# Performance work log

Hardware: AMD Instinct MI355X
Metric: run time of the kernel (lower is better)

The kernel has to match this reference:

```python
import jax, jax.numpy as jnp
import numpy as np

N = 50000      # nodes
E = 800000     # edges (before self-loops)
G = 64         # graphs
F_IN = 128
HID = 64
HEADS = 2
OUT = 10
NEG_SLOPE = 0.2


def setup_inputs() -> dict:
    key = jax.random.key(0)
    ks = jax.random.split(key, 12)
    x = jax.random.normal(ks[0], (N, F_IN), dtype=jnp.float32)
    edge_index = jax.random.randint(ks[1], (2, E), 0, N, dtype=jnp.int64)
    batch = jnp.sort(jax.random.randint(ks[2], (N,), 0, G, dtype=jnp.int64))
    s = 0.1
    params = {
        "W1": jax.random.normal(ks[3], (F_IN, HEADS * HID), dtype=jnp.float32) * s,
        "att_src1": jax.random.normal(ks[4], (HEADS, HID), dtype=jnp.float32) * s,
        "att_dst1": jax.random.normal(ks[5], (HEADS, HID), dtype=jnp.float32) * s,
        "b1": jnp.zeros((HEADS * HID,), dtype=jnp.float32),
        "W2": jax.random.normal(ks[6], (HEADS * HID, HEADS * HID), dtype=jnp.float32) * s,
        "att_src2": jax.random.normal(ks[7], (HEADS, HID), dtype=jnp.float32) * s,
        "att_dst2": jax.random.normal(ks[8], (HEADS, HID), dtype=jnp.float32) * s,
        "b2": jnp.zeros((HEADS * HID,), dtype=jnp.float32),
        "Wl": jax.random.normal(ks[9], (HEADS * HID, OUT), dtype=jnp.float32) * s,
        "bl": jnp.zeros((OUT,), dtype=jnp.float32),
    }
    return {"x": x, "edge_index": edge_index, "batch": batch, **params}


def gat_conv(x, W, att_src, att_dst, bias, src, dst):
    # x: [N, Fin]; W: [Fin, H*C]
    h = (x @ W).reshape(N, HEADS, HID)                      # [N, H, C]
    a_src = jnp.sum(h * att_src, axis=-1)                   # [N, H]
    a_dst = jnp.sum(h * att_dst, axis=-1)                   # [N, H]
    alpha = jax.nn.leaky_relu(a_src[src] + a_dst[dst], NEG_SLOPE)  # [Etot, H]
    # segment softmax over incoming edges of each dst node
    m = jax.ops.segment_max(alpha, dst, num_segments=N)     # [N, H]
    alpha = jnp.exp(alpha - m[dst])
    denom = jax.ops.segment_sum(alpha, dst, num_segments=N)
    alpha = alpha / (denom[dst] + 1e-16)
    out = jax.ops.segment_sum(alpha[:, :, None] * h[src], dst, num_segments=N)
    return out.reshape(N, HEADS * HID) + bias


def reference(x, edge_index, batch, W1, att_src1, att_dst1, b1,
              W2, att_src2, att_dst2, b2, Wl, bl):
    # PyG GATConv default: add self-loops
    loop = jnp.arange(N, dtype=edge_index.dtype)
    src = jnp.concatenate([edge_index[0], loop])
    dst = jnp.concatenate([edge_index[1], loop])

    h = jax.nn.relu(gat_conv(x, W1, att_src1, att_dst1, b1, src, dst))
    h = jax.nn.relu(gat_conv(h, W2, att_src2, att_dst2, b2, src, dst))

    # global_mean_pool over graphs
    sums = jax.ops.segment_sum(h, batch, num_segments=G)        # [G, H*C]
    cnts = jax.ops.segment_sum(jnp.ones((N,), h.dtype), batch, num_segments=G)
    pooled = sums / jnp.maximum(cnts, 1.0)[:, None]
    return pooled @ Wl + bl                                      # [G, OUT]
```

## Files before the change

kernel.cpp:

```cpp
#include <hip/hip_runtime.h>
#include <hip/hip_fp16.h>
#include <math.h>

#define N_NODES 50000
#define N_EDGES 800000
#define ETOT    850000
#define GRAPHS  64
#define FIN     128
#define HC      128
#define OUTF    10
#define NEG     0.2f

#define NBUCK   196
#define BCAP    8192
#define EPT     8

using half8  = __attribute__((ext_vector_type(8))) _Float16;
using float4v = __attribute__((ext_vector_type(4))) float;

__global__ void initk(int* tails, float* sums) {
    int i = blockIdx.x * 256 + threadIdx.x;
    if (i < NBUCK) tails[i] = 0;
    if (i < GRAPHS * HC) sums[i] = 0.f;
}

__global__ void wconv(const float* __restrict__ W1, const float* __restrict__ W2,
                      _Float16* __restrict__ WT1, _Float16* __restrict__ WT2) {
    int t = blockIdx.x * 256 + threadIdx.x;
    if (t < 16384) {
        int n = t >> 7, k = t & 127;
        WT1[t] = (_Float16)W1[k * 128 + n];
        WT2[t] = (_Float16)W2[k * 128 + n];
    }
}

__global__ __launch_bounds__(256) void bucketA(const int* __restrict__ ei,
                                               int* __restrict__ tails,
                                               int* __restrict__ bdata) {
    __shared__ int hist[NBUCK];
    __shared__ int lbase[NBUCK];
    int t = threadIdx.x;
    int e0 = blockIdx.x * (256 * EPT);
    for (int i = t; i < NBUCK; i += 256) hist[i] = 0;
    __syncthreads();

    int bb[EPT], pk[EPT], rk[EPT];
#pragma unroll
    for (int i = 0; i < EPT; ++i) {
        int e = e0 + i * 256 + t;
        bb[i] = -1;
        if (e < ETOT) {
            int s, d;
            if (e < N_EDGES) { s = ei[e]; d = ei[N_EDGES + e]; }
            else             { s = d = e - N_EDGES; }
            bb[i] = d >> 8;
            pk[i] = s | ((d & 255) << 16);
            rk[i] = atomicAdd(&hist[bb[i]], 1);
        }
    }
    __syncthreads();
    for (int i = t; i < NBUCK; i += 256)
        lbase[i] = atomicAdd(&tails[i], hist[i]);
    __syncthreads();
#pragma unroll
    for (int i = 0; i < EPT; ++i)
        if (bb[i] >= 0) bdata[bb[i] * BCAP + lbase[bb[i]] + rk[i]] = pk[i];
}

__global__ void scanBuckets(const int* __restrict__ tails,
                            int* __restrict__ csrBase,
                            int* __restrict__ rowptr) {
    __shared__ int sh[256];
    int t = threadIdx.x;
    int c = (t < NBUCK) ? tails[t] : 0;
    sh[t] = c;
    __syncthreads();
    for (int off = 1; off < 256; off <<= 1) {
        int add = (t >= off) ? sh[t - off] : 0;
        __syncthreads();
        sh[t] += add;
        __syncthreads();
    }
    if (t < NBUCK) csrBase[t] = sh[t] - c;
    if (t == NBUCK - 1) rowptr[N_NODES] = sh[t];
}

__global__ __launch_bounds__(256) void bucketB(const int* __restrict__ bdata,
                                               const int* __restrict__ tails,
                                               const int* __restrict__ csrBase,
                                               int* __restrict__ rowptr,
                                               int* __restrict__ csr) {
    __shared__ int hist[256];
    __shared__ int scanws[256];
    int b = blockIdx.x;
    int t = threadIdx.x;
    int nodes0 = b << 8;
    int nnodes = min(256, N_NODES - nodes0);
    int cnt  = tails[b];
    int base = csrBase[b];
    const int* bd = &bdata[b * BCAP];

    hist[t] = 0;
    __syncthreads();
    for (int j = t; j < cnt; j += 256) atomicAdd(&hist[bd[j] >> 16], 1);
    __syncthreads();
    scanws[t] = hist[t];
    __syncthreads();
    for (int off = 1; off < 256; off <<= 1) {
        int add = (t >= off) ? scanws[t - off] : 0;
        __syncthreads();
        scanws[t] += add;
        __syncthreads();
    }
    int excl = scanws[t] - hist[t];
    if (t < nnodes) rowptr[nodes0 + t] = base + excl;
    __syncthreads();
    hist[t] = excl;
    __syncthreads();
    for (int j = t; j < cnt; j += 256) {
        int pkv = bd[j];
        int pos = atomicAdd(&hist[pkv >> 16], 1);
        csr[base + pos] = pkv & 0xFFFF;
    }
}

template<bool FP32IN>
__global__ __launch_bounds__(256) void gemmMFMA(const void* __restrict__ Xin,
                                                const _Float16* __restrict__ WT,
                                                const float* __restrict__ att_s,
                                                const float* __restrict__ att_d,
                                                _Float16* __restrict__ H16,
                                                float2* __restrict__ a_src,
                                                float2* __restrict__ a_dst) {
    __shared__ _Float16 wt[128][128];
    int t = threadIdx.x;

    for (int i = t; i < 128 * 16; i += 256) {
        int n = i >> 4, ch = i & 15;
        int k0 = ch * 8;
        half8 v = *(const half8*)&WT[n * 128 + k0];
        *(half8*)&wt[n][k0 ^ ((n & 7) << 3)] = v;
    }

    int w = t >> 6, lane = t & 63;
    int hi = lane >> 4, l16 = lane & 15;
    int rbase = blockIdx.x * 64 + w * 16;
    int arow = min(rbase + l16, N_NODES - 1);

    half8 a[4];
    if (FP32IN) {
        const float* X = (const float*)Xin;
#pragma unroll
        for (int kb = 0; kb < 4; ++kb) {
            int k0 = kb * 32 + hi * 8;
            float4 x0 = *(const float4*)&X[(size_t)arow * 128 + k0];
            float4 x1 = *(const float4*)&X[(size_t)arow * 128 + k0 + 4];
            half8 v;
            v[0] = (_Float16)x0.x; v[1] = (_Float16)x0.y;
            v[2] = (_Float16)x0.z; v[3] = (_Float16)x0.w;
            v[4] = (_Float16)x1.x; v[5] = (_Float16)x1.y;
            v[6] = (_Float16)x1.z; v[7] = (_Float16)x1.w;
            a[kb] = v;
        }
    } else {
        const _Float16* X = (const _Float16*)Xin;
#pragma unroll
        for (int kb = 0; kb < 4; ++kb)
            a[kb] = *(const half8*)&X[(size_t)arow * 128 + kb * 32 + hi * 8];
    }

    __syncthreads();

    float4v acc[8];
#pragma unroll
    for (int ct = 0; ct < 8; ++ct) {
        float4v c = {0.f, 0.f, 0.f, 0.f};
        int n = ct * 16 + l16;
#pragma unroll
        for (int kb = 0; kb < 4; ++kb) {
            int k0 = (kb * 32 + hi * 8) ^ ((n & 7) << 3);
            half8 b = *(const half8*)&wt[n][k0];
            c = __builtin_amdgcn_mfma_f32_16x16x32_f16(a[kb], b, c, 0, 0, 0);
        }
        acc[ct] = c;
    }

    int grow0 = rbase + hi * 4;
#pragma unroll
    for (int ct = 0; ct < 8; ++ct) {
#pragma unroll
        for (int r = 0; r < 4; ++r) {
            int grow = grow0 + r;
            if (grow < N_NODES)
                H16[(size_t)grow * 128 + ct * 16 + l16] = (_Float16)acc[ct][r];
        }
    }

    float as_[8], ad_[8];
#pragma unroll
    for (int ct = 0; ct < 8; ++ct) {
        as_[ct] = att_s[ct * 16 + l16];
        ad_[ct] = att_d[ct * 16 + l16];
    }
#pragma unroll
    for (int r = 0; r < 4; ++r) {
        float s0 = 0.f, s1 = 0.f, d0 = 0.f, d1 = 0.f;
#pragma unroll
        for (int ct = 0; ct < 4; ++ct) { s0 += acc[ct][r] * as_[ct]; d0 += acc[ct][r] * ad_[ct]; }
#pragma unroll
        for (int ct = 4; ct < 8; ++ct) { s1 += acc[ct][r] * as_[ct]; d1 += acc[ct][r] * ad_[ct]; }
        for (int off = 1; off < 16; off <<= 1) {
            s0 += __shfl_xor(s0, off); s1 += __shfl_xor(s1, off);
            d0 += __shfl_xor(d0, off); d1 += __shfl_xor(d1, off);
        }
        int grow = grow0 + r;
        if (l16 == 0 && grow < N_NODES) {
            a_src[grow] = make_float2(s0, s1);
            a_dst[grow] = make_float2(d0, d1);
        }
    }
}

__device__ __forceinline__ float leaky(float x) { return x > 0.f ? x : NEG * x; }

__global__ __launch_bounds__(256) void aggk(const __half* __restrict__ H16,
                                            const float2* __restrict__ a_src,
                                            const float2* __restrict__ a_dst,
                                            const int* __restrict__ rowptr,
                                            const int* __restrict__ csr,
                                            const float* __restrict__ bias,
                                            float* __restrict__ outp,
                                            _Float16* __restrict__ out16) {
    int wid = (blockIdx.x * 256 + threadIdx.x) >> 6;
    int lane = threadIdx.x & 63;
    if (wid >= N_NODES) return;
    int rbeg = rowptr[wid], rend = rowptr[wid + 1];
    float2 ad = a_dst[wid];

    int grp = lane >> 4;
    int gl  = lane & 15;
    int head = gl >> 3;
    float adh = head ? ad.y : ad.x;
    int f = gl * 8;

    float acc[8] = {0.f, 0.f, 0.f, 0.f, 0.f, 0.f, 0.f, 0.f};
    float denom = 0.f;
#pragma unroll 2
    for (int j = rbeg + grp; j < rend; j += 4) {
        int s = csr[j];
        float2 as = a_src[s];
        float w = __expf(leaky((head ? as.y : as.x) + adh));
        uint4 raw = *(const uint4*)&H16[(size_t)s * 128 + f];
        float2 f0 = __half22float2(*(__half2*)&raw.x);
        float2 f1 = __half22float2(*(__half2*)&raw.y);
        float2 f2 = __half22float2(*(__half2*)&raw.z);
        float2 f3 = __half22float2(*(__half2*)&raw.w);
        acc[0] += w * f0.x; acc[1] += w * f0.y;
        acc[2] += w * f1.x; acc[3] += w * f1.y;
        acc[4] += w * f2.x; acc[5] += w * f2.y;
        acc[6] += w * f3.x; acc[7] += w * f3.y;
        denom += w;
    }
#pragma unroll
    for (int off = 16; off <= 32; off <<= 1) {
#pragma unroll
        for (int i = 0; i < 8; ++i) acc[i] += __shfl_xor(acc[i], off);
        denom += __shfl_xor(denom, off);
    }

    if (grp == 0) {
        float inv = 1.f / (denom + 1e-16f);
        float4 bb0 = *(const float4*)&bias[f];
        float4 bb1 = *(const float4*)&bias[f + 4];
        float o[8];
        o[0] = fmaxf(acc[0] * inv + bb0.x, 0.f);
        o[1] = fmaxf(acc[1] * inv + bb0.y, 0.f);
        o[2] = fmaxf(acc[2] * inv + bb0.z, 0.f);
        o[3] = fmaxf(acc[3] * inv + bb0.w, 0.f);
        o[4] = fmaxf(acc[4] * inv + bb1.x, 0.f);
        o[5] = fmaxf(acc[5] * inv + bb1.y, 0.f);
        o[6] = fmaxf(acc[6] * inv + bb1.z, 0.f);
        o[7] = fmaxf(acc[7] * inv + bb1.w, 0.f);
        *(float4*)&outp[(size_t)wid * 128 + f]     = make_float4(o[0], o[1], o[2], o[3]);
        *(float4*)&outp[(size_t)wid * 128 + f + 4] = make_float4(o[4], o[5], o[6], o[7]);
        half8 h;
#pragma unroll
        for (int i = 0; i < 8; ++i) h[i] = (_Float16)o[i];
        *(half8*)&out16[(size_t)wid * 128 + f] = h;
    }
}

__global__ void countk(const int* __restrict__ batch, int* cnt) {
    int g = threadIdx.x;
    if (g >= GRAPHS) return;
    int lo = 0, hi = N_NODES;
    while (lo < hi) { int mid = (lo + hi) >> 1; if (batch[mid] < g) lo = mid + 1; else hi = mid; }
    int lb = lo;
    lo = 0; hi = N_NODES;
    while (lo < hi) { int mid = (lo + hi) >> 1; if (batch[mid] < g + 1) lo = mid + 1; else hi = mid; }
    cnt[g] = lo - lb;
}

__global__ void poolk(const float* __restrict__ H, const int* __restrict__ batch,
                      float* __restrict__ sums) {
    int f = threadIdx.x;
    int n0 = blockIdx.x * 64;
    if (n0 >= N_NODES) return;
    int n1 = min(n0 + 64, N_NODES);
    int g = batch[n0];
    float run = 0.f;
    for (int n = n0; n < n1; ++n) {
        int gn = batch[n];
        if (gn != g) { atomicAdd(&sums[g * 128 + f], run); run = 0.f; g = gn; }
        run += H[(size_t)n * 128 + f];
    }
    atomicAdd(&sums[g * 128 + f], run);
}

__global__ void finalk(const float* __restrict__ sums, const int* __restrict__ cnt,
                       const float* __restrict__ Wl, const float* __restrict__ bl,
                       float* __restrict__ out) {
    int t = threadIdx.x;
    if (t >= GRAPHS * OUTF) return;
    int g = t / OUTF, o = t % OUTF;
    float inv = 1.f / fmaxf((float)cnt[g], 1.f);
    float acc = 0.f;
#pragma unroll 8
    for (int k = 0; k < 128; ++k) acc += sums[g * 128 + k] * Wl[k * OUTF + o];
    out[t] = acc * inv + bl[o];
}

extern "C" void kernel_launch(void* const* d_in, const int* in_sizes, int n_in,
                              void* d_out, int out_size, void* d_ws, size_t ws_size,
                              hipStream_t stream) {
    const float* x        = (const float*)d_in[0];
    const int*   ei       = (const int*)d_in[1];
    const int*   batch    = (const int*)d_in[2];
    const float* W1       = (const float*)d_in[3];
    const float* att_src1 = (const float*)d_in[4];
    const float* att_dst1 = (const float*)d_in[5];
    const float* b1       = (const float*)d_in[6];
    const float* W2       = (const float*)d_in[7];
    const float* att_src2 = (const float*)d_in[8];
    const float* att_dst2 = (const float*)d_in[9];
    const float* b2       = (const float*)d_in[10];
    const float* Wl       = (const float*)d_in[11];
    const float* bl       = (const float*)d_in[12];
    float* out = (float*)d_out;

    size_t off = 0;
    auto alloc = [&](size_t bytes) -> void* {
        void* p = (char*)d_ws + off;
        off = (off + bytes + 255) & ~(size_t)255;
        return p;
    };
    float*    B       = (float*)alloc((size_t)N_NODES * 128 * 4);
    _Float16* H16     = (_Float16*)alloc((size_t)N_NODES * 128 * 2);
    _Float16* B16     = (_Float16*)alloc((size_t)N_NODES * 128 * 2);
    _Float16* WT1     = (_Float16*)alloc(16384 * 2);
    _Float16* WT2     = (_Float16*)alloc(16384 * 2);
    float2*   a_src   = (float2*)alloc((size_t)N_NODES * 8);
    float2*   a_dst   = (float2*)alloc((size_t)N_NODES * 8);
    int*      bdata   = (int*)alloc((size_t)NBUCK * BCAP * 4);
    int*      tails   = (int*)alloc(NBUCK * 4);
    int*      csrBase = (int*)alloc(NBUCK * 4);
    int*      rowptr  = (int*)alloc((size_t)(N_NODES + 1) * 4);
    int*      csr     = (int*)alloc((size_t)ETOT * 4);
    float*    sums    = (float*)alloc((size_t)GRAPHS * HC * 4);
    int*      cnt     = (int*)alloc(GRAPHS * 4);

    initk<<<32, 256, 0, stream>>>(tails, sums);
    wconv<<<64, 256, 0, stream>>>(W1, W2, WT1, WT2);
    bucketA<<<(ETOT + 2047) / 2048, 256, 0, stream>>>(ei, tails, bdata);
    scanBuckets<<<1, 256, 0, stream>>>(tails, csrBase, rowptr);
    bucketB<<<NBUCK, 256, 0, stream>>>(bdata, tails, csrBase, rowptr, csr);

    const int gemmBlocks = (N_NODES + 63) / 64;
    const int waveBlocks = (N_NODES * 64 + 255) / 256;

    gemmMFMA<true><<<gemmBlocks, 256, 0, stream>>>(x, WT1, att_src1, att_dst1,
                                                   H16, a_src, a_dst);
    aggk<<<waveBlocks, 256, 0, stream>>>((const __half*)H16, a_src, a_dst,
                                         rowptr, csr, b1, B, B16);

    gemmMFMA<false><<<gemmBlocks, 256, 0, stream>>>(B16, WT2, att_src2, att_dst2,
                                                    H16, a_src, a_dst);
    aggk<<<waveBlocks, 256, 0, stream>>>((const __half*)H16, a_src, a_dst,
                                         rowptr, csr, b2, B, B16);

    countk<<<1, 64, 0, stream>>>(batch, cnt);
    poolk<<<(N_NODES + 63) / 64, 128, 0, stream>>>(B, batch, sums);
    finalk<<<1, 640, 0, stream>>>(sums, cnt, Wl, bl, out);
}
```

Baseline: 183.5 us.

## Drop fp32 node output, widen per-lane features, prefetch edge index in aggregation

The aggregation kernel no longer writes a float32 copy of node features; pooling now reads the fp16 buffer instead. Each lane now handles 16 features with two 16-byte loads, so 8 edges are processed in parallel per wavefront rather than 4, and the next source index is prefetched one iteration ahead. This removes 25.6 MB of fp32 writes per layer plus the matching pooling reads, and puts more edges in flight per wave. The cost is an extra shuffle-reduction stage, higher register use, and pooling now summing fp16-rounded values.

```diff
diff --git a/kernel.cpp b/kernel.cpp
--- a/kernel.cpp
+++ b/kernel.cpp
@@ -15,7 +15,7 @@
 #define BCAP    8192
 #define EPT     8
 
-using half8  = __attribute__((ext_vector_type(8))) _Float16;
+using half8   = __attribute__((ext_vector_type(8))) _Float16;
 using float4v = __attribute__((ext_vector_type(4))) float;
 
 __global__ void initk(int* tails, float* sums) {
@@ -229,7 +229,6 @@
                                             const int* __restrict__ rowptr,
                                             const int* __restrict__ csr,
                                             const float* __restrict__ bias,
-                                            float* __restrict__ outp,
                                             _Float16* __restrict__ out16) {
     int wid = (blockIdx.x * 256 + threadIdx.x) >> 6;
     int lane = threadIdx.x & 63;
@@ -237,56 +236,61 @@
     int rbeg = rowptr[wid], rend = rowptr[wid + 1];
     float2 ad = a_dst[wid];
 
-    int grp = lane >> 4;
-    int gl  = lane & 15;
-    int head = gl >> 3;
+    int grp = lane >> 3;
+    int gl  = lane & 7;
+    int head = gl >> 2;
     float adh = head ? ad.y : ad.x;
-    int f = gl * 8;
-
-    float acc[8] = {0.f, 0.f, 0.f, 0.f, 0.f, 0.f, 0.f, 0.f};
+    int f = gl * 16;
+
+    float acc[16];
+#pragma unroll
+    for (int i = 0; i < 16; ++i) acc[i] = 0.f;
     float denom = 0.f;
-#pragma unroll 2
-    for (int j = rbeg + grp; j < rend; j += 4) {
-        int s = csr[j];
+
+    int j = rbeg + grp;
+    int sNext = (j < rend) ? csr[j] : 0;
+    for (; j < rend; j += 8) {
+        int s = sNext;
+        int jn = j + 8;
+        if (jn < rend) sNext = csr[jn];
         float2 as = a_src[s];
-        float w = __expf(leaky((head ? as.y : as.x) + adh));
-        uint4 raw = *(const uint4*)&H16[(size_t)s * 128 + f];
-        float2 f0 = __half22float2(*(__half2*)&raw.x);
-        float2 f1 = __half22float2(*(__half2*)&raw.y);
-        float2 f2 = __half22float2(*(__half2*)&raw.z);
-        float2 f3 = __half22float2(*(__half2*)&raw.w);
-        acc[0] += w * f0.x; acc[1] += w * f0.y;
-        acc[2] += w * f1.x; acc[3] += w * f1.y;
-        acc[4] += w * f2.x; acc[5] += w * f2.y;
-        acc[6] += w * f3.x; acc[7] += w * f3.y;
-        denom += w;
-    }
-#pragma unroll
-    for (int off = 16; off <= 32; off <<= 1) {
-#pragma unroll
-        for (int i = 0; i < 8; ++i) acc[i] += __shfl_xor(acc[i], off);
+        float wgt = __expf(leaky((head ? as.y : as.x) + adh));
+        const uint4* hp = (const uint4*)&H16[(size_t)s * 128 + f];
+        uint4 r0 = hp[0];
+        uint4 r1 = hp[1];
+        float2 p;
+        p = __half22float2(*(__half2*)&r0.x); acc[0] += wgt * p.x; acc[1] += wgt * p.y;
+        p = __half22float2(*(__half2*)&r0.y); acc[2] += wgt * p.x; acc[3] += wgt * p.y;
+        p = __half22float2(*(__half2*)&r0.z); acc[4] += wgt * p.x; acc[5] += wgt * p.y;
+        p = __half22float2(*(__half2*)&r0.w); acc[6] += wgt * p.x; acc[7] += wgt * p.y;
+        p = __half22float2(*(__half2*)&r1.x); acc[8] += wgt * p.x; acc[9] += wgt * p.y;
+        p = __half22float2(*(__half2*)&r1.y); acc[10] += wgt * p.x; acc[11] += wgt * p.y;
+        p = __half22float2(*(__half2*)&r1.z); acc[12] += wgt * p.x; acc[13] += wgt * p.y;
+        p = __half22float2(*(__half2*)&r1.w); acc[14] += wgt * p.x; acc[15] += wgt * p.y;
+        denom += wgt;
+    }
+#pragma unroll
+    for (int off = 8; off <= 32; off <<= 1) {
+#pragma unroll
+        for (int i = 0; i < 16; ++i) acc[i] += __shfl_xor(acc[i], off);
         denom += __shfl_xor(denom, off);
     }
 
     if (grp == 0) {
         float inv = 1.f / (denom + 1e-16f);
-        float4 bb0 = *(const float4*)&bias[f];
-        float4 bb1 = *(const float4*)&bias[f + 4];
-        float o[8];
-        o[0] = fmaxf(acc[0] * inv + bb0.x, 0.f);
-        o[1] = fmaxf(acc[1] * inv + bb0.y, 0.f);
-        o[2] = fmaxf(acc[2] * inv + bb0.z, 0.f);
-        o[3] = fmaxf(acc[3] * inv + bb0.w, 0.f);
-        o[4] = fmaxf(acc[4] * inv + bb1.x, 0.f);
-        o[5] = fmaxf(acc[5] * inv + bb1.y, 0.f);
-        o[6] = fmaxf(acc[6] * inv + bb1.z, 0.f);
-        o[7] = fmaxf(acc[7] * inv + bb1.w, 0.f);
-        *(float4*)&outp[(size_t)wid * 128 + f]     = make_float4(o[0], o[1], o[2], o[3]);
-        *(float4*)&outp[(size_t)wid * 128 + f + 4] = make_float4(o[4], o[5], o[6], o[7]);
-        half8 h;
-#pragma unroll
-        for (int i = 0; i < 8; ++i) h[i] = (_Float16)o[i];
-        *(half8*)&out16[(size_t)wid * 128 + f] = h;
+        half8 h0, h1;
+#pragma unroll
+        for (int i = 0; i < 8; ++i) {
+            float o = fmaxf(acc[i] * inv + bias[f + i], 0.f);
+            h0[i] = (_Float16)o;
+        }
+#pragma unroll
+        for (int i = 0; i < 8; ++i) {
+            float o = fmaxf(acc[8 + i] * inv + bias[f + 8 + i], 0.f);
+            h1[i] = (_Float16)o;
+        }
+        *(half8*)&out16[(size_t)wid * 128 + f]     = h0;
+        *(half8*)&out16[(size_t)wid * 128 + f + 8] = h1;
     }
 }
 
@@ -301,7 +305,7 @@
     cnt[g] = lo - lb;
 }
 
-__global__ void poolk(const float* __restrict__ H, const int* __restrict__ batch,
+__global__ void poolk(const _Float16* __restrict__ H, const int* __restrict__ batch,
                       float* __restrict__ sums) {
     int f = threadIdx.x;
     int n0 = blockIdx.x * 64;
@@ -312,7 +316,7 @@
     for (int n = n0; n < n1; ++n) {
         int gn = batch[n];
         if (gn != g) { atomicAdd(&sums[g * 128 + f], run); run = 0.f; g = gn; }
-        run += H[(size_t)n * 128 + f];
+        run += (float)H[(size_t)n * 128 + f];
     }
     atomicAdd(&sums[g * 128 + f], run);
 }
@@ -354,7 +358,6 @@
         off = (off + bytes + 255) & ~(size_t)255;
         return p;
     };
-    float*    B       = (float*)alloc((size_t)N_NODES * 128 * 4);
     _Float16* H16     = (_Float16*)alloc((size_t)N_NODES * 128 * 2);
     _Float16* B16     = (_Float16*)alloc((size_t)N_NODES * 128 * 2);
     _Float16* WT1     = (_Float16*)alloc(16384 * 2);
@@ -381,14 +384,14 @@
     gemmMFMA<true><<<gemmBlocks, 256, 0, stream>>>(x, WT1, att_src1, att_dst1,
                                                    H16, a_src, a_dst);
     aggk<<<waveBlocks, 256, 0, stream>>>((const __half*)H16, a_src, a_dst,
-                                         rowptr, csr, b1, B, B16);
+                                         rowptr, csr, b1, B16);
 
     gemmMFMA<false><<<gemmBlocks, 256, 0, stream>>>(B16, WT2, att_src2, att_dst2,
                                                     H16, a_src, a_dst);
     aggk<<<waveBlocks, 256, 0, stream>>>((const __half*)H16, a_src, a_dst,
-                                         rowptr, csr, b2, B, B16);
+                                         rowptr, csr, b2, B16);
 
     countk<<<1, 64, 0, stream>>>(batch, cnt);
-    poolk<<<(N_NODES + 63) / 64, 128, 0, stream>>>(B, batch, sums);
+    poolk<<<(N_NODES + 63) / 64, 128, 0, stream>>>(B16, batch, sums);
     finalk<<<1, 640, 0, stream>>>(sums, cnt, Wl, bl, out);
 }
```

Result: faster. 173.7 us (-5.4%).
